# Kernel optimization log

Measured on AMD Instinct MI355X. Metric: run time of the kernel, lower is better.

Reference implementation:

```python
import jax, jax.numpy as jnp
import numpy as np

NUM_HEADS = 16
THETA = 10000.0


def _rope(x, pos, theta):
    # x: [b, h, s, d_k] with d_k even; rotate interleaved pairs (even, odd)
    d = x.shape[-1]
    inv_freq = theta ** (-jnp.arange(0, d, 2, dtype=jnp.float32) / d)  # [d/2]
    ang = pos.astype(jnp.float32)[:, None] * inv_freq                  # [s, d/2]
    cos = jnp.cos(ang)[None, None]                                     # [1,1,s,d/2]
    sin = jnp.sin(ang)[None, None]
    x1 = x[..., 0::2]
    x2 = x[..., 1::2]
    r1 = x1 * cos - x2 * sin
    r2 = x1 * sin + x2 * cos
    return jnp.stack([r1, r2], axis=-1).reshape(x.shape)


def setup_inputs() -> dict:
    key = jax.random.key(0)
    ks = jax.random.split(key, 5)
    B, S, D = 2, 2048, 1024
    x = jax.random.normal(ks[0], (B, S, D), dtype=jnp.float32)
    scale = 0.02
    Wq = jax.random.normal(ks[1], (D, D), dtype=jnp.float32) * scale
    Wk = jax.random.normal(ks[2], (D, D), dtype=jnp.float32) * scale
    Wv = jax.random.normal(ks[3], (D, D), dtype=jnp.float32) * scale
    Wo = jax.random.normal(ks[4], (D, D), dtype=jnp.float32) * scale
    return {"x": x, "Wq": Wq, "Wk": Wk, "Wv": Wv, "Wo": Wo}


def reference(x, Wq, Wk, Wv, Wo):
    B, S, D = x.shape
    H = NUM_HEADS
    dk = D // H
    # QKV projections (bias-free Linear: y = x @ W^T, W is [out, in])
    q = (x @ Wq.T).reshape(B, S, H, dk).transpose(0, 2, 1, 3)  # [b,h,s,dk]
    k = (x @ Wk.T).reshape(B, S, H, dk).transpose(0, 2, 1, 3)
    v = (x @ Wv.T).reshape(B, S, H, dk).transpose(0, 2, 1, 3)
    pos = jnp.arange(S)
    q = _rope(q, pos, THETA)
    k = _rope(k, pos, THETA)
    # naive masked SDPA, causal mask
    scores = jnp.einsum('bhqd,bhkd->bhqk', q, k) / (dk ** 0.5)
    causal = jnp.tril(jnp.ones((S, S), dtype=bool))
    scores = jnp.where(causal, scores, -jnp.inf)
    attn = jax.nn.softmax(scores, axis=-1)
    out = jnp.einsum('bhqk,bhkd->bhqd', attn, v)
    out = out.transpose(0, 2, 1, 3).reshape(B, S, D)
    return out @ Wo.T
```

## Files before the change

### kernel.cpp

```cpp
#include <hip/hip_runtime.h>
#include <hip/hip_bf16.h>
#include <stdint.h>

typedef __bf16 bf16;
typedef __bf16 bf16x8 __attribute__((ext_vector_type(8)));
typedef float f32x4 __attribute__((ext_vector_type(4)));
typedef float f32x16 __attribute__((ext_vector_type(16)));

#define B_ 2
#define S_ 2048
#define D_ 1024
#define H_ 16
#define DK 64
#define M_ 4096

__device__ __forceinline__ void gload_lds16(const void* g, void* l) {
  __builtin_amdgcn_global_load_lds(
      (const __attribute__((address_space(1))) uint32_t*)(uintptr_t)g,
      (__attribute__((address_space(3))) uint32_t*)(uintptr_t)l, 16, 0, 0);
}

__device__ __forceinline__ uint32_t pkbf(float a, float b) {
  union { uint32_t u; struct { bf16 x, y; } s; } r;
  r.s.x = (bf16)a; r.s.y = (bf16)b;
  return r.u;
}

struct alignas(8) B4s { bf16 a, b, c, d; };

__global__ __launch_bounds__(256) void cvt_all_kernel(
    const float* __restrict__ x, const float* __restrict__ wq, const float* __restrict__ wk,
    const float* __restrict__ wv, const float* __restrict__ wo,
    bf16* __restrict__ xb, bf16* __restrict__ wqb, bf16* __restrict__ wkb,
    bf16* __restrict__ wvb, bf16* __restrict__ wob) {
  int i = blockIdx.x * 256 + threadIdx.x;
  const float* src;
  bf16* dst;
  int off;
  if (i < 1048576) { src = x; dst = xb; off = i; }
  else if (i < 1310720) { src = wq; dst = wqb; off = i - 1048576; }
  else if (i < 1572864) { src = wk; dst = wkb; off = i - 1310720; }
  else if (i < 1835008) { src = wv; dst = wvb; off = i - 1572864; }
  else { src = wo; dst = wob; off = i - 1835008; }
  float4 v = reinterpret_cast<const float4*>(src)[off];
  B4s o{(bf16)v.x, (bf16)v.y, (bf16)v.z, (bf16)v.w};
  reinterpret_cast<B4s*>(dst)[off] = o;
}

template <int MODE>
__global__ __launch_bounds__(256) void gemm_kernel(
    const bf16* __restrict__ A,
    const bf16* __restrict__ W0, const bf16* __restrict__ W1, const bf16* __restrict__ W2,
    bf16* __restrict__ q_out, bf16* __restrict__ k_out, bf16* __restrict__ v_out,
    float* __restrict__ c_out) {
  constexpr int BK = 32;
  __shared__ bf16 Alds[128 * BK];
  __shared__ bf16 Blds[128 * BK];
  const int tid = threadIdx.x;
  const int w = tid >> 6, l = tid & 63;
  const int lr = l & 15, lg = l >> 4;
  const int m0 = blockIdx.y * 128;
  const int nt = blockIdx.x;
  const bf16* W;
  int n0;
  if (MODE == 0) {
    W = (nt >> 3) == 0 ? W0 : ((nt >> 3) == 1 ? W1 : W2);
    n0 = (nt & 7) * 128;
  } else {
    W = W0;
    n0 = nt * 128;
  }
  const int K = 1024;
  const int wm = (w >> 1) * 64, wn = (w & 1) * 64;
  const int srow = w * 16 + (l >> 2);
  const int scol = (l & 3) * 8;
  f32x4 acc[4][4] = {};
  for (int k0 = 0; k0 < K; k0 += BK) {
    gload_lds16(A + (size_t)(m0 + srow) * K + k0 + scol, Alds + (w * 16) * BK);
    gload_lds16(A + (size_t)(m0 + 64 + srow) * K + k0 + scol, Alds + (64 + w * 16) * BK);
    gload_lds16(W + (size_t)(n0 + srow) * K + k0 + scol, Blds + (w * 16) * BK);
    gload_lds16(W + (size_t)(n0 + 64 + srow) * K + k0 + scol, Blds + (64 + w * 16) * BK);
    __syncthreads();
    bf16x8 af[4], bfr[4];
#pragma unroll
    for (int f = 0; f < 4; ++f) {
      af[f]  = *reinterpret_cast<const bf16x8*>(Alds + (wm + f * 16 + lr) * BK + lg * 8);
      bfr[f] = *reinterpret_cast<const bf16x8*>(Blds + (wn + f * 16 + lr) * BK + lg * 8);
    }
#pragma unroll
    for (int fm = 0; fm < 4; ++fm)
#pragma unroll
      for (int fn = 0; fn < 4; ++fn)
        acc[fm][fn] = __builtin_amdgcn_mfma_f32_16x16x32_bf16(af[fm], bfr[fn], acc[fm][fn], 0, 0, 0);
    __syncthreads();
  }
#pragma unroll
  for (int fm = 0; fm < 4; ++fm)
#pragma unroll
    for (int fn = 0; fn < 4; ++fn)
#pragma unroll
      for (int r = 0; r < 4; ++r) {
        int m = m0 + wm + fm * 16 + lg * 4 + r;
        int n = n0 + wn + fn * 16 + lr;
        float v = acc[fm][fn][r];
        if (MODE == 0) {
          bf16* dst = (nt >> 3) == 0 ? q_out : ((nt >> 3) == 1 ? k_out : v_out);
          int h = n >> 6, d = n & 63;
          int b = m >> 11, s = m & 2047;
          dst[(((size_t)b * H_ + h) * S_ + s) * DK + d] = (bf16)v;
        } else {
          c_out[(size_t)m * D_ + n] = v;
        }
      }
}

__global__ __launch_bounds__(256) void rope_kernel(bf16* __restrict__ Q, bf16* __restrict__ K) {
  const int NG = 32 * 2048 * 8;
  int idx = blockIdx.x * 256 + threadIdx.x;
  bf16* X = Q;
  float sc = 0.18033688f;
  if (idx >= NG) { X = K; idx -= NG; sc = 1.0f; }
  int g = idx & 7;
  int s = (idx >> 3) & 2047;
  int bh = idx >> 14;
  size_t off = ((size_t)bh * S_ + s) * DK + g * 8;
  bf16x8 v = *reinterpret_cast<const bf16x8*>(X + off);
  bf16x8 o;
  const float c0 = -0.4152410118609203f;
  float fs = (float)s;
#pragma unroll
  for (int p = 0; p < 4; ++p) {
    int i = g * 4 + p;
    float ang = fs * exp2f((float)i * c0);
    float sn = __sinf(ang), cs = __cosf(ang);
    float x1 = (float)v[2 * p], x2 = (float)v[2 * p + 1];
    o[2 * p]     = (bf16)((x1 * cs - x2 * sn) * sc);
    o[2 * p + 1] = (bf16)((x1 * sn + x2 * cs) * sc);
  }
  *reinterpret_cast<bf16x8*>(X + off) = o;
}

__global__ __launch_bounds__(256, 4) void attn_kernel(
    const bf16* __restrict__ Q, const bf16* __restrict__ K, const bf16* __restrict__ V,
    bf16* __restrict__ O) {
  __shared__ __align__(16) char smem[24576];
  bf16* KldsB = (bf16*)smem;
  bf16* Vt = (bf16*)smem + 8192;
  float* MG = (float*)smem;
  const int tid = threadIdx.x;
  const int w = tid >> 6, l = tid & 63;
  const int ql = l & 31, h = l >> 5;
  const int kh = w >> 1, qh = w & 1;
  const int qt = 31 - (int)(blockIdx.x >> 5);
  const int bh = blockIdx.x & 31;
  const size_t base = (size_t)bh * S_ * DK;

  const size_t qrow = base + (size_t)(qt * 64 + qh * 32 + ql) * DK;
  bf16x8 qf[4];
#pragma unroll
  for (int t = 0; t < 4; ++t)
    qf[t] = *reinterpret_cast<const bf16x8*>(Q + qrow + t * 16 + h * 8);

  float m_run = -INFINITY, l_run = 0.f;
  f32x16 o0 = {}, o1 = {};

  auto stageK = [&](int kt, int p) {
#pragma unroll
    for (int c = 0; c < 2; ++c) {
      int row = c * 32 + w * 8 + (l >> 3);
      int col = ((l & 7) * 8) ^ ((row & 7) * 8);
      gload_lds16(K + base + (size_t)(kt * 64 + row) * DK + col,
                  KldsB + p * 4096 + c * 2048 + w * 512);
    }
  };
  auto loadV = [&](int kt, bf16x8 (&pv)[2]) {
    const bf16* vp = V + base + (size_t)(kt * 64 + l) * DK + w * 16;
    pv[0] = *reinterpret_cast<const bf16x8*>(vp);
    pv[1] = *reinterpret_cast<const bf16x8*>(vp + 8);
  };
  auto writeV = [&](const bf16x8 (&pv)[2]) {
#pragma unroll
    for (int j = 0; j < 8; ++j) {
      Vt[(w * 16 + j) * 64 + (l ^ (j * 8))] = pv[0][j];
      Vt[(w * 16 + 8 + j) * 64 + (l ^ (j * 8))] = pv[1][j];
    }
  };

  {
    stageK(0, 0);
    bf16x8 pv[2];
    loadV(0, pv);
    writeV(pv);
  }
  __syncthreads();

  const int swzd = (ql & 7) * 8;
  const int keyA = kh * 32 + ql;
  const int limq = qh * 32 + ql;
  bf16x8 pvv[2];

  for (int kt = 0; kt <= qt; ++kt) {
    const int p = kt & 1;
    const bool pre = kt < qt;
    const bool lastt = (kt == qt);
    const bool skipw = lastt && (kh == 1) && (qh == 0);
    if (pre) {
      stageK(kt + 1, p ^ 1);
      loadV(kt + 1, pvv);
    }
    if (!skipw) {
      f32x16 ss = {};
      __builtin_amdgcn_s_setprio(1);
#pragma unroll
      for (int t = 0; t < 4; ++t) {
        bf16x8 kf = *reinterpret_cast<const bf16x8*>(
            KldsB + p * 4096 + keyA * 64 + ((t * 16 + h * 8) ^ ((keyA & 7) * 8)));
        ss = __builtin_amdgcn_mfma_f32_32x32x16_bf16(kf, qf[t], ss, 0, 0, 0);
      }
      __builtin_amdgcn_s_setprio(0);
      if (lastt) {
#pragma unroll
        for (int r = 0; r < 16; ++r) {
          int kl = kh * 32 + (r & 3) + 8 * (r >> 2) + 4 * h;
          if (kl > limq) ss[r] = -INFINITY;
        }
      }
      float tmax = -INFINITY;
#pragma unroll
      for (int r = 0; r < 16; ++r) tmax = fmaxf(tmax, ss[r]);
      tmax = fmaxf(tmax, __shfl_xor(tmax, 32));
      if (!__all(tmax <= m_run + 11.0f)) {
        float m_new = fmaxf(m_run, tmax);
        float sf = exp2f(m_run - m_new);
        l_run *= sf;
#pragma unroll
        for (int r = 0; r < 16; ++r) {
          float sfr = __shfl(sf, (r & 3) + 8 * (r >> 2) + 4 * h);
          o0[r] *= sfr;
          o1[r] *= sfr;
        }
        m_run = m_new;
      }
      float ts = 0.f;
#pragma unroll
      for (int r = 0; r < 16; ++r) {
        float pp = exp2f(ss[r] - m_run);
        ss[r] = pp;
        ts += pp;
      }
      ts += __shfl_xor(ts, 32);
      l_run += ts;
      uint32_t Wq_[4][2];
#pragma unroll
      for (int g = 0; g < 4; ++g) {
        Wq_[g][0] = pkbf(ss[4 * g + 0], ss[4 * g + 1]);
        Wq_[g][1] = pkbf(ss[4 * g + 2], ss[4 * g + 3]);
      }
      __builtin_amdgcn_s_setprio(1);
#pragma unroll
      for (int ks = 0; ks < 2; ++ks) {
        uint32_t a0 = Wq_[2 * ks][0], a1 = Wq_[2 * ks][1];
        uint32_t b0 = Wq_[2 * ks + 1][0], b1 = Wq_[2 * ks + 1][1];
        uint32_t sxa0 = (uint32_t)__shfl_xor((int)a0, 32);
        uint32_t sxa1 = (uint32_t)__shfl_xor((int)a1, 32);
        uint32_t sxb0 = (uint32_t)__shfl_xor((int)b0, 32);
        uint32_t sxb1 = (uint32_t)__shfl_xor((int)b1, 32);
        union { uint32_t u[4]; bf16x8 v; } pa;
        pa.u[0] = h ? sxb0 : a0;
        pa.u[1] = h ? sxb1 : a1;
        pa.u[2] = h ? b0 : sxa0;
        pa.u[3] = h ? b1 : sxa1;
        int col = (kh * 32 + ks * 16 + h * 8) ^ swzd;
        bf16x8 v0 = *reinterpret_cast<const bf16x8*>(&Vt[ql * 64 + col]);
        bf16x8 v1 = *reinterpret_cast<const bf16x8*>(&Vt[(32 + ql) * 64 + col]);
        o0 = __builtin_amdgcn_mfma_f32_32x32x16_bf16(pa.v, v0, o0, 0, 0, 0);
        o1 = __builtin_amdgcn_mfma_f32_32x32x16_bf16(pa.v, v1, o1, 0, 0, 0);
      }
      __builtin_amdgcn_s_setprio(0);
    }
    __syncthreads();
    if (pre) writeV(pvv);
    __syncthreads();
  }

  if (kh == 1) {
    int off = (qh * 64 + l) * 34;
    MG[off] = m_run;
    MG[off + 1] = l_run;
#pragma unroll
    for (int r = 0; r < 16; ++r) {
      MG[off + 2 + r] = o0[r];
      MG[off + 18 + r] = o1[r];
    }
  }
  __syncthreads();
  if (kh == 0) {
    int off = (qh * 64 + l) * 34;
    float m1 = MG[off], l1 = MG[off + 1];
    float m = fmaxf(m_run, m1);
    float s0 = exp2f(m_run - m), s1 = exp2f(m1 - m);
    float inv = 1.0f / (l_run * s0 + l1 * s1);
    const int b = bh >> 4, hd = bh & 15;
#pragma unroll
    for (int r = 0; r < 16; ++r) {
      int rowl = (r & 3) + 8 * (r >> 2) + 4 * h;
      float s0r = __shfl(s0, rowl);
      float s1r = __shfl(s1, rowl);
      float invr = __shfl(inv, rowl);
      int qr = qt * 64 + qh * 32 + rowl;
      size_t ooff = ((size_t)b * S_ + qr) * D_ + hd * 64;
      O[ooff + ql] = (bf16)((o0[r] * s0r + MG[off + 2 + r] * s1r) * invr);
      O[ooff + 32 + ql] = (bf16)((o1[r] * s0r + MG[off + 18 + r] * s1r) * invr);
    }
  }
}

extern "C" void kernel_launch(void* const* d_in, const int* in_sizes, int n_in,
                              void* d_out, int out_size, void* d_ws, size_t ws_size,
                              hipStream_t stream) {
  const float* x  = (const float*)d_in[0];
  const float* Wq = (const float*)d_in[1];
  const float* Wk = (const float*)d_in[2];
  const float* Wv = (const float*)d_in[3];
  const float* Wo = (const float*)d_in[4];
  float* out = (float*)d_out;
  char* ws = (char*)d_ws;

  bf16* xb  = (bf16*)(ws + ((size_t)0 << 20));
  bf16* wqb = (bf16*)(ws + ((size_t)8 << 20));
  bf16* wkb = (bf16*)(ws + ((size_t)10 << 20));
  bf16* wvb = (bf16*)(ws + ((size_t)12 << 20));
  bf16* wob = (bf16*)(ws + ((size_t)14 << 20));
  bf16* Qb  = (bf16*)(ws + ((size_t)16 << 20));
  bf16* Kb  = (bf16*)(ws + ((size_t)24 << 20));
  bf16* Vb  = (bf16*)(ws + ((size_t)32 << 20));
  bf16* Ob  = (bf16*)(ws + ((size_t)40 << 20));

  cvt_all_kernel<<<8192, 256, 0, stream>>>(x, Wq, Wk, Wv, Wo, xb, wqb, wkb, wvb, wob);
  gemm_kernel<0><<<dim3(24, 32), 256, 0, stream>>>(xb, wqb, wkb, wvb, Qb, Kb, Vb, nullptr);
  rope_kernel<<<4096, 256, 0, stream>>>(Qb, Kb);
  attn_kernel<<<1024, 256, 0, stream>>>(Qb, Kb, Vb, Ob);
  gemm_kernel<1><<<dim3(8, 32), 256, 0, stream>>>(Ob, wob, nullptr, nullptr, nullptr, nullptr,
                                                  nullptr, out);
}
```

Baseline: 129.6 us.

## Fuse RoPE into QKV GEMM epilogue and triple-buffer K in attention

Applies the rotary embedding and the Q scaling inside the QKV projection GEMM epilogue, using a lane shuffle to fetch each pair partner. This removes the separate rope kernel launch and its read/write pass over Q and K. The attention kernel also moves to a three-slot K ring and double-buffered V in LDS, prefetching K two tiles ahead. That replaces the two __syncthreads per tile with one barrier guarded by explicit waitcnt. LDS use rises from 24 KB to 40 KB, which may lower occupancy at the declared launch bounds of 4 blocks.

```diff
diff --git a/kernel.cpp b/kernel.cpp
--- a/kernel.cpp
+++ b/kernel.cpp
@@ -94,6 +94,16 @@
         acc[fm][fn] = __builtin_amdgcn_mfma_f32_16x16x32_bf16(af[fm], bfr[fn], acc[fm][fn], 0, 0, 0);
     __syncthreads();
   }
+  const int rt = (MODE == 0) ? (nt >> 3) : 0;
+  const bool dorope = (MODE == 0) && (rt < 2);
+  const float qsc = (rt == 0) ? 0.18033688f : 1.0f;
+  const float c0 = -0.4152410118609203f;
+  float invf[4];
+  if (dorope) {
+#pragma unroll
+    for (int fn = 0; fn < 4; ++fn)
+      invf[fn] = exp2f((float)(((wn + fn * 16 + lr) & 63) >> 1) * c0);
+  }
 #pragma unroll
   for (int fm = 0; fm < 4; ++fm)
 #pragma unroll
@@ -104,7 +114,15 @@
         int n = n0 + wn + fn * 16 + lr;
         float v = acc[fm][fn][r];
         if (MODE == 0) {
-          bf16* dst = (nt >> 3) == 0 ? q_out : ((nt >> 3) == 1 ? k_out : v_out);
+          if (dorope) {
+            float pp = __shfl_xor(v, 1);
+            int s = m & 2047;
+            float ang = (float)s * invf[fn];
+            float sn = __sinf(ang), cs = __cosf(ang);
+            v = (lr & 1) ? (pp * sn + v * cs) : (v * cs - pp * sn);
+            v *= qsc;
+          }
+          bf16* dst = rt == 0 ? q_out : (rt == 1 ? k_out : v_out);
           int h = n >> 6, d = n & 63;
           int b = m >> 11, s = m & 2047;
           dst[(((size_t)b * H_ + h) * S_ + s) * DK + d] = (bf16)v;
@@ -114,38 +132,12 @@
       }
 }
 
-__global__ __launch_bounds__(256) void rope_kernel(bf16* __restrict__ Q, bf16* __restrict__ K) {
-  const int NG = 32 * 2048 * 8;
-  int idx = blockIdx.x * 256 + threadIdx.x;
-  bf16* X = Q;
-  float sc = 0.18033688f;
-  if (idx >= NG) { X = K; idx -= NG; sc = 1.0f; }
-  int g = idx & 7;
-  int s = (idx >> 3) & 2047;
-  int bh = idx >> 14;
-  size_t off = ((size_t)bh * S_ + s) * DK + g * 8;
-  bf16x8 v = *reinterpret_cast<const bf16x8*>(X + off);
-  bf16x8 o;
-  const float c0 = -0.4152410118609203f;
-  float fs = (float)s;
-#pragma unroll
-  for (int p = 0; p < 4; ++p) {
-    int i = g * 4 + p;
-    float ang = fs * exp2f((float)i * c0);
-    float sn = __sinf(ang), cs = __cosf(ang);
-    float x1 = (float)v[2 * p], x2 = (float)v[2 * p + 1];
-    o[2 * p]     = (bf16)((x1 * cs - x2 * sn) * sc);
-    o[2 * p + 1] = (bf16)((x1 * sn + x2 * cs) * sc);
-  }
-  *reinterpret_cast<bf16x8*>(X + off) = o;
-}
-
 __global__ __launch_bounds__(256, 4) void attn_kernel(
     const bf16* __restrict__ Q, const bf16* __restrict__ K, const bf16* __restrict__ V,
     bf16* __restrict__ O) {
-  __shared__ __align__(16) char smem[24576];
-  bf16* KldsB = (bf16*)smem;
-  bf16* Vt = (bf16*)smem + 8192;
+  __shared__ __align__(16) char smem[40960];
+  bf16* K3 = (bf16*)smem;
+  bf16* Vt2 = (bf16*)smem + 12288;
   float* MG = (float*)smem;
   const int tid = threadIdx.x;
   const int w = tid >> 6, l = tid & 63;
@@ -164,13 +156,13 @@
   float m_run = -INFINITY, l_run = 0.f;
   f32x16 o0 = {}, o1 = {};
 
-  auto stageK = [&](int kt, int p) {
+  auto stageK = [&](int kt, int buf) {
 #pragma unroll
     for (int c = 0; c < 2; ++c) {
       int row = c * 32 + w * 8 + (l >> 3);
       int col = ((l & 7) * 8) ^ ((row & 7) * 8);
       gload_lds16(K + base + (size_t)(kt * 64 + row) * DK + col,
-                  KldsB + p * 4096 + c * 2048 + w * 512);
+                  K3 + buf * 4096 + c * 2048 + w * 512);
     }
   };
   auto loadV = [&](int kt, bf16x8 (&pv)[2]) {
@@ -178,7 +170,8 @@
     pv[0] = *reinterpret_cast<const bf16x8*>(vp);
     pv[1] = *reinterpret_cast<const bf16x8*>(vp + 8);
   };
-  auto writeV = [&](const bf16x8 (&pv)[2]) {
+  auto writeV = [&](int vb, const bf16x8 (&pv)[2]) {
+    bf16* Vt = Vt2 + vb * 4096;
 #pragma unroll
     for (int j = 0; j < 8; ++j) {
       Vt[(w * 16 + j) * 64 + (l ^ (j * 8))] = pv[0][j];
@@ -187,34 +180,43 @@
   };
 
   {
-    stageK(0, 0);
     bf16x8 pv[2];
     loadV(0, pv);
-    writeV(pv);
-  }
-  __syncthreads();
+    stageK(0, 0);
+    if (qt >= 1) stageK(1, 1);
+    writeV(0, pv);
+    if (qt >= 1) {
+      asm volatile("s_waitcnt vmcnt(2)" ::: "memory");
+    } else {
+      asm volatile("s_waitcnt vmcnt(0)" ::: "memory");
+    }
+    asm volatile("s_waitcnt lgkmcnt(0)" ::: "memory");
+    __builtin_amdgcn_sched_barrier(0);
+    __builtin_amdgcn_s_barrier();
+    __builtin_amdgcn_sched_barrier(0);
+  }
 
   const int swzd = (ql & 7) * 8;
   const int keyA = kh * 32 + ql;
   const int limq = qh * 32 + ql;
   bf16x8 pvv[2];
+  int kb = 0, kb2 = 2;
 
   for (int kt = 0; kt <= qt; ++kt) {
-    const int p = kt & 1;
+    const int vb = kt & 1;
     const bool pre = kt < qt;
+    const bool pre2 = kt + 2 <= qt;
     const bool lastt = (kt == qt);
     const bool skipw = lastt && (kh == 1) && (qh == 0);
-    if (pre) {
-      stageK(kt + 1, p ^ 1);
-      loadV(kt + 1, pvv);
-    }
+    if (pre) loadV(kt + 1, pvv);
+    if (pre2) stageK(kt + 2, kb2);
     if (!skipw) {
       f32x16 ss = {};
       __builtin_amdgcn_s_setprio(1);
 #pragma unroll
       for (int t = 0; t < 4; ++t) {
         bf16x8 kf = *reinterpret_cast<const bf16x8*>(
-            KldsB + p * 4096 + keyA * 64 + ((t * 16 + h * 8) ^ ((keyA & 7) * 8)));
+            K3 + kb * 4096 + keyA * 64 + ((t * 16 + h * 8) ^ ((keyA & 7) * 8)));
         ss = __builtin_amdgcn_mfma_f32_32x32x16_bf16(kf, qf[t], ss, 0, 0, 0);
       }
       __builtin_amdgcn_s_setprio(0);
@@ -271,6 +273,7 @@
         pa.u[2] = h ? b0 : sxa0;
         pa.u[3] = h ? b1 : sxa1;
         int col = (kh * 32 + ks * 16 + h * 8) ^ swzd;
+        const bf16* Vt = Vt2 + vb * 4096;
         bf16x8 v0 = *reinterpret_cast<const bf16x8*>(&Vt[ql * 64 + col]);
         bf16x8 v1 = *reinterpret_cast<const bf16x8*>(&Vt[(32 + ql) * 64 + col]);
         o0 = __builtin_amdgcn_mfma_f32_32x32x16_bf16(pa.v, v0, o0, 0, 0, 0);
@@ -278,9 +281,14 @@
       }
       __builtin_amdgcn_s_setprio(0);
     }
-    __syncthreads();
-    if (pre) writeV(pvv);
-    __syncthreads();
+    if (pre) writeV(vb ^ 1, pvv);
+    asm volatile("s_waitcnt vmcnt(2)" ::: "memory");
+    asm volatile("s_waitcnt lgkmcnt(0)" ::: "memory");
+    __builtin_amdgcn_sched_barrier(0);
+    __builtin_amdgcn_s_barrier();
+    __builtin_amdgcn_sched_barrier(0);
+    kb = (kb == 2) ? 0 : kb + 1;
+    kb2 = (kb2 == 2) ? 0 : kb2 + 1;
   }
 
   if (kh == 1) {
@@ -338,7 +346,6 @@
 
   cvt_all_kernel<<<8192, 256, 0, stream>>>(x, Wq, Wk, Wv, Wo, xb, wqb, wkb, wvb, wob);
   gemm_kernel<0><<<dim3(24, 32), 256, 0, stream>>>(xb, wqb, wkb, wvb, Qb, Kb, Vb, nullptr);
-  rope_kernel<<<4096, 256, 0, stream>>>(Qb, Kb);
   attn_kernel<<<1024, 256, 0, stream>>>(Qb, Kb, Vb, Ob);
   gemm_kernel<1><<<dim3(8, 32), 256, 0, stream>>>(Ob, wob, nullptr, nullptr, nullptr, nullptr,
                                                   nullptr, out);
```

Result: slower. 143.8 us (+11.0%).
